# Kernel tuning notes

Hardware: AMD Instinct MI355X
Metric: run time of the kernel (lower is better)

Reference implementation:

```python
import jax, jax.numpy as jnp
import numpy as np

EPS = 1e-10


def setup_inputs() -> dict:
    key = jax.random.key(0)
    k1, k2, k3 = jax.random.split(key, 3)
    B, c = 65536, 64
    xyz = jax.random.normal(k1, (B, 3, 1), dtype=jnp.float32)          # group centers
    xyz_group = xyz + 0.1 * jax.random.normal(k2, (B, 3, c), dtype=jnp.float32)  # neighbor points
    r_lrf = 0.2 + 0.8 * jax.random.uniform(k3, (B,), dtype=jnp.float32)  # per-group support radius
    return {"xyz": xyz, "xyz_group": xyz_group, "r_lrf": r_lrf}


def reference(xyz, xyz_group, r_lrf):
    # xyz: [B,3,1] center; xyz_group: [B,3,c] neighbors; r_lrf: [B]
    B, _, c = xyz_group.shape
    x = xyz - xyz_group                                   # [B,3,c]
    xxt = jnp.einsum('bic,bjc->bij', x, x) / c            # [B,3,3] covariance
    _, _, vh = jnp.linalg.svd(xxt)                        # vh: [B,3,3]
    v_last = vh[:, -1, :]                                 # [B,3] smallest singular vector (torch v[...,-1])

    # sign disambiguation (no-grad in the original)
    center_proj = jnp.einsum('bi,bic->bc', v_last, x)     # [B,c]
    sum_ = (center_proj > 0.001).sum(-1) - (center_proj < -0.001).sum(-1)  # [B]
    sign = jax.lax.stop_gradient(1.0 - 2.0 * (sum_ < 0).astype(jnp.float32))  # [B]

    zp = sign[:, None] * v_last                           # [B,3] z axis
    x = -x                                                # x *= -1 in original
    norm = jnp.einsum('bi,bic->bc', zp, x)                # [B,c] projection onto zp
    vi = x - zp[:, :, None] * norm[:, None, :]            # [B,3,c] in-plane component
    x_l2 = jnp.sqrt(jnp.sum(x * x, axis=1))               # [B,c]
    alpha = (r_lrf[:, None] - x_l2) ** 2                  # [B,c]
    beta = norm * norm                                    # [B,c]
    vi_c = jnp.einsum('bc,bic->bi', alpha * beta, vi)     # [B,3] weighted sum
    xp = vi_c / (jnp.sqrt(jnp.sum(vi_c * vi_c, axis=1, keepdims=True)) + EPS)  # [B,3] x axis
    yp = jnp.cross(xp, zp)                                # [B,3] y axis
    lrf = jnp.stack([xp, yp, zp], axis=2)                 # [B,3,3] columns = axes
    out = jnp.einsum('bij,bic->bjc', lrf, (xyz_group - xyz) / r_lrf[:, None, None])  # lrf^T @ _out_xp
    return out


if __name__ == '__main__':
    o = reference(**setup_inputs())
    print(o.shape)
```

## Files before the change

### kernel.cpp

```cpp
#include <hip/hip_runtime.h>


#define DEVFN static __device__ __forceinline__

DEVFN float frcp(float x) { return __builtin_amdgcn_rcpf(x); }
DEVFN float frsq(float x) { return __builtin_amdgcn_rsqf(x); }


DEVFN float slapy2f(float x, float y) {
#pragma clang fp contract(off)
  float xa = fabsf(x), ya = fabsf(y);
  float w = fmaxf(xa, ya);
  float z = fminf(xa, ya);
  if (z == 0.0f) return w;
  float q = z / w;
  return w * sqrtf(fmaf(q, q, 1.0f));
}

DEVFN float snrm2_2f(float a, float b) {
  double da = (double)a, db = (double)b;
  return (float)sqrt(da * da + db * db);
}

DEVFN void slartgf(float f, float g, float &cs, float &sn, float &r) {
#pragma clang fp contract(off)
  if (g == 0.0f) { cs = 1.0f; sn = 0.0f; r = f; return; }
  if (f == 0.0f) { cs = 0.0f; sn = copysignf(1.0f, g); r = fabsf(g); return; }
  float f1 = fabsf(f), g1 = fabsf(g);
  const float rtmin = 0x1p-63f;
  const float rtmax = 6.5219089e18f;
  if (f1 > rtmin && f1 < rtmax && g1 > rtmin && g1 < rtmax) {
    float d = sqrtf(fmaf(f, f, g * g));
    cs = f1 / d;
    r = copysignf(d, f);
    sn = g / r;
  } else {
    const float safmin = 0x1p-126f;
    const float safmax = 0x1p+126f;
    float u = fminf(safmax, fmaxf(safmin, fmaxf(f1, g1)));
    float fs = f / u, gs = g / u;
    float d = sqrtf(fmaf(fs, fs, gs * gs));
    cs = fabsf(fs) / d;
    r = copysignf(d, f);
    sn = gs / r;
    r = r * u;
  }
}

DEVFN void slas2f(float f, float g, float h, float &ssmin, float &ssmax) {
#pragma clang fp contract(off)
  float fa = fabsf(f), ga = fabsf(g), ha = fabsf(h);
  float fhmn = fminf(fa, ha), fhmx = fmaxf(fa, ha);
  if (fhmn == 0.0f) {
    ssmin = 0.0f;
    if (fhmx == 0.0f) {
      ssmax = ga;
    } else {
      float mx = fmaxf(fhmx, ga), mn = fminf(fhmx, ga);
      float q = mn / mx;
      ssmax = mx * sqrtf(fmaf(q, q, 1.0f));
    }
  } else {
    if (ga < fhmx) {
      float as = 1.0f + fhmn / fhmx;
      float at = (fhmx - fhmn) / fhmx;
      float qq = ga / fhmx;
      float au = qq * qq;
      float c = 2.0f / (sqrtf(fmaf(as, as, au)) + sqrtf(fmaf(at, at, au)));
      ssmin = fhmn * c;
      ssmax = fhmx / c;
    } else {
      float au = fhmx / ga;
      if (au == 0.0f) {
        ssmin = (fhmn * fhmx) / ga;
        ssmax = ga;
      } else {
        float as = 1.0f + fhmn / fhmx;
        float at = (fhmx - fhmn) / fhmx;
        float q1 = as * au, q2 = at * au;
        float c = 1.0f / (sqrtf(fmaf(q1, q1, 1.0f)) + sqrtf(fmaf(q2, q2, 1.0f)));
        ssmin = (fhmn * c) * au;
        ssmin = ssmin + ssmin;
        ssmax = ga / (c + c);
      }
    }
  }
}

DEVFN void slasv2f(float f, float g, float h, float &ssmin, float &ssmax,
                   float &snr, float &csr, float &snl, float &csl) {
#pragma clang fp contract(off)
  const float eps = 0x1p-24f;
  float ft = f, fa = fabsf(f), ht = h, ha = fabsf(h);
  int pmax = 1;
  bool swp = (ha > fa);
  if (swp) {
    pmax = 3;
    float tmp = ft; ft = ht; ht = tmp;
    tmp = fa; fa = ha; ha = tmp;
  }
  float gt = g, ga = fabsf(g);
  float clt = 0.0f, crt = 0.0f, slt = 0.0f, srt = 0.0f;
  if (ga == 0.0f) {
    ssmin = ha; ssmax = fa;
    clt = 1.0f; crt = 1.0f; slt = 0.0f; srt = 0.0f;
  } else {
    bool gasmal = true;
    if (ga > fa) {
      pmax = 2;
      if ((fa / ga) < eps) {
        gasmal = false;
        ssmax = ga;
        if (ha > 1.0f) ssmin = fa / (ga / ha);
        else ssmin = (fa / ga) * ha;
        clt = 1.0f; slt = ht / gt; srt = 1.0f; crt = ft / gt;
      }
    }
    if (gasmal) {
      float dd = fa - ha;
      float l;
      if (dd == fa) l = 1.0f;
      else l = dd / fa;
      float m = gt / ft;
      float t = 2.0f - l;
      float s = sqrtf(fmaf(m, m, t * t));
      float r;
      if (l == 0.0f) r = fabsf(m);
      else r = sqrtf(fmaf(m, m, l * l));
      float a = 0.5f * (s + r);
      ssmin = ha / a;
      ssmax = fa * a;
      float mm = m * m;
      if (mm == 0.0f) {
        if (l == 0.0f) t = copysignf(2.0f, ft) * copysignf(1.0f, gt);
        else t = gt / copysignf(dd, ft) + m / t;
      } else {
        t = (m / (s + t) + m / (r + l)) * (1.0f + a);
      }
      float l2 = sqrtf(fmaf(t, t, 4.0f));
      crt = 2.0f / l2;
      srt = t / l2;
      clt = fmaf(srt, m, crt) / a;
      slt = (ht / ft) * srt / a;
    }
  }
  if (swp) { csl = srt; snl = crt; csr = slt; snr = clt; }
  else { csl = clt; snl = slt; csr = crt; snr = srt; }
  float tsign = 0.0f;
  if (pmax == 1) tsign = copysignf(1.0f, csr) * copysignf(1.0f, csl) * copysignf(1.0f, f);
  if (pmax == 2) tsign = copysignf(1.0f, snr) * copysignf(1.0f, csl) * copysignf(1.0f, g);
  if (pmax == 3) tsign = copysignf(1.0f, snr) * copysignf(1.0f, snl) * copysignf(1.0f, h);
  ssmax = copysignf(ssmax, tsign);
  ssmin = copysignf(ssmin, tsign * copysignf(1.0f, f) * copysignf(1.0f, h));
}

#define GROT(hi1, hi2, hi3, lo1, lo2, lo3, ct_, st_)          \
  do {                                                        \
    float c__ = (ct_), s__ = (st_);                           \
    if (c__ != 1.0f || s__ != 0.0f) {                         \
      float t_;                                               \
      t_ = hi1; hi1 = fmaf(c__, t_, -(s__ * lo1)); lo1 = fmaf(s__, t_, c__ * lo1); \
      t_ = hi2; hi2 = fmaf(c__, t_, -(s__ * lo2)); lo2 = fmaf(s__, t_, c__ * lo2); \
      t_ = hi3; hi3 = fmaf(c__, t_, -(s__ * lo3)); lo3 = fmaf(s__, t_, c__ * lo3); \
    }                                                         \
  } while (0)

#define ROT2X2(lo1, lo2, lo3, hi1, hi2, hi3, cr_, sr_)        \
  do {                                                        \
    float xx_, yy_, st_;                                      \
    xx_ = lo1; yy_ = hi1; st_ = fmaf(cr_, xx_, sr_ * yy_);    \
    hi1 = fmaf(cr_, yy_, -(sr_ * xx_)); lo1 = st_;            \
    xx_ = lo2; yy_ = hi2; st_ = fmaf(cr_, xx_, sr_ * yy_);    \
    hi2 = fmaf(cr_, yy_, -(sr_ * xx_)); lo2 = st_;            \
    xx_ = lo3; yy_ = hi3; st_ = fmaf(cr_, xx_, sr_ * yy_);    \
    hi3 = fmaf(cr_, yy_, -(sr_ * xx_)); lo3 = st_;            \
  } while (0)

#define VSWAP(a, b) { float t_ = (a); (a) = (b); (b) = t_; }

static __device__ void svd3_vlast(float c00, float c01, float c02,
                                  float c11, float c12, float c22,
                                  float vout[3]) {
#pragma clang fp contract(off)
  float a11 = c00, a12 = c01, a13 = c02;
  float a21 = c01, a22 = c11, a23 = c12;
  float a31 = c02, a32 = c12, a33 = c22;
  float d1, d2, d3, e1, e2;
  float taup1 = 0.0f, g2 = 0.0f;

  {
    float xnorm = snrm2_2f(a21, a31);
    if (xnorm == 0.0f) {
      d1 = a11;
    } else {
      float beta = -copysignf(slapy2f(a11, xnorm), a11);
      float tauq1 = (beta - a11) / beta;
      float sc = 1.0f / (a11 - beta);
      float v2 = a21 * sc, v3 = a31 * sc;
      d1 = beta;
      float w2 = fmaf(a32, v3, a22 * v2);
      float w3 = fmaf(a33, v3, a23 * v2);
      w2 = w2 + a12;
      w3 = w3 + a13;
      a12 = fmaf(-tauq1, w2, a12);
      a13 = fmaf(-tauq1, w3, a13);
      float t2 = -tauq1 * w2;
      float t3 = -tauq1 * w3;
      a22 = fmaf(v2, t2, a22); a32 = fmaf(v3, t2, a32);
      a23 = fmaf(v2, t3, a23); a33 = fmaf(v3, t3, a33);
    }
  }
  {
    float xnorm = fabsf(a13);
    if (xnorm == 0.0f) {
      e1 = a12;
    } else {
      float beta = -copysignf(slapy2f(a12, xnorm), a12);
      taup1 = (beta - a12) / beta;
      g2 = a13 * (1.0f / (a12 - beta));
      e1 = beta;
      float w2 = a23 * g2;
      float w3 = a33 * g2;
      w2 = w2 + a22;
      w3 = w3 + a32;
      a22 = fmaf(-taup1, w2, a22);
      a32 = fmaf(-taup1, w3, a32);
      float tg = -taup1 * g2;
      a23 = fmaf(w2, tg, a23);
      a33 = fmaf(w3, tg, a33);
    }
  }
  {
    float xnorm = fabsf(a32);
    if (xnorm == 0.0f) {
      d2 = a22;
    } else {
      float beta = -copysignf(slapy2f(a22, xnorm), a22);
      float tauq2 = (beta - a22) / beta;
      float h3 = a32 * (1.0f / (a22 - beta));
      d2 = beta;
      float w = a33 * h3;
      w = w + a23;
      a23 = fmaf(-tauq2, w, a23);
      float tw = -tauq2 * w;
      a33 = fmaf(h3, tw, a33);
    }
  }
  e2 = a23;
  d3 = a33;

  float vt11 = 1.0f, vt12 = 0.0f, vt13 = 0.0f;
  float vt21 = 0.0f, vt22 = 1.0f, vt23 = 0.0f;
  float vt31 = 0.0f, vt32 = 0.0f, vt33 = 1.0f;

  const float eps = 0x1p-24f;
  const float unfl = 0x1p-126f;
  const float tol = 10.0f * eps;
  float thresh;
  {
    float sminoa = fabsf(d1);
    if (sminoa != 0.0f) {
      float mu = sminoa;
      mu = fabsf(d2) * (mu / (mu + fabsf(e1)));
      sminoa = fminf(sminoa, mu);
      if (sminoa != 0.0f) {
        mu = fabsf(d3) * (mu / (mu + fabsf(e2)));
        sminoa = fminf(sminoa, mu);
      }
    }
    sminoa = sminoa / sqrtf(3.0f);
    thresh = fmaxf(tol * sminoa, 6.0f * (3.0f * (3.0f * unfl)));
  }
  int mq = 3;
  int iterq = -1, iterdivn = 0;
  const int maxitdivn = 18;
  int oldll = -1, oldm = -1, idir = 0;
  float sminl = 0.0f;
  int guard = 0;

  while (true) {
    if (mq <= 1) break;
    if (++guard > 300) break;
    if (iterq >= 3) {
      iterq -= 3;
      iterdivn += 1;
      if (iterdivn >= maxitdivn) break;
    }
    if (mq == 2) {
      if (fabsf(e1) <= thresh) { e1 = 0.0f; mq = 1; continue; }
      float sigmn, sigmx, sinr, cosr, sinl, cosl;
      slasv2f(d1, e1, d2, sigmn, sigmx, sinr, cosr, sinl, cosl);
      d1 = sigmx; e1 = 0.0f; d2 = sigmn;
      ROT2X2(vt11, vt12, vt13, vt21, vt22, vt23, cosr, sinr);
      mq = 0;
      continue;
    }
    float smax = fabsf(d3);
    if (fabsf(e2) <= thresh) { e2 = 0.0f; mq = 2; continue; }
    smax = fmaxf(fmaxf(smax, fabsf(d2)), fabsf(e2));
    if (fabsf(e1) <= thresh) {
      e1 = 0.0f;
      float sigmn, sigmx, sinr, cosr, sinl, cosl;
      slasv2f(d2, e2, d3, sigmn, sigmx, sinr, cosr, sinl, cosl);
      d2 = sigmx; e2 = 0.0f; d3 = sigmn;
      ROT2X2(vt21, vt22, vt23, vt31, vt32, vt33, cosr, sinr);
      mq = 1;
      continue;
    }
    smax = fmaxf(fmaxf(smax, fabsf(d1)), fabsf(e1));
    if (1 > oldm || 3 < oldll)
      idir = (fabsf(d1) >= fabsf(d3)) ? 1 : 2;
    bool back = false;
    if (idir == 1) {
      if (fabsf(e2) <= tol * fabsf(d3)) { e2 = 0.0f; continue; }
      float mu = fabsf(d1);
      sminl = mu;
      if (fabsf(e1) <= tol * mu) { e1 = 0.0f; back = true; }
      else {
        mu = fabsf(d2) * (mu / (mu + fabsf(e1)));
        sminl = fminf(sminl, mu);
        if (fabsf(e2) <= tol * mu) { e2 = 0.0f; back = true; }
        else {
          mu = fabsf(d3) * (mu / (mu + fabsf(e2)));
          sminl = fminf(sminl, mu);
        }
      }
    } else {
      if (fabsf(e1) <= tol * fabsf(d1)) { e1 = 0.0f; continue; }
      float mu = fabsf(d3);
      sminl = mu;
      if (fabsf(e2) <= tol * mu) { e2 = 0.0f; back = true; }
      else {
        mu = fabsf(d2) * (mu / (mu + fabsf(e2)));
        sminl = fminf(sminl, mu);
        if (fabsf(e1) <= tol * mu) { e1 = 0.0f; back = true; }
        else {
          mu = fabsf(d1) * (mu / (mu + fabsf(e1)));
          sminl = fminf(sminl, mu);
        }
      }
    }
    if (back) continue;
    oldll = 1;
    oldm = 3;
    float shift = 0.0f;
    if (!((3.0f * tol) * (sminl / smax) <= fmaxf(eps, 0.01f * tol))) {
      float sll, rdum;
      if (idir == 1) { sll = fabsf(d1); slas2f(d2, e2, d3, shift, rdum); }
      else { sll = fabsf(d3); slas2f(d1, e1, d2, shift, rdum); }
      if (sll > 0.0f) {
        float q = shift / sll;
        if (q * q < eps) shift = 0.0f;
      }
    }
    iterq += 2;
    float rc0, rc1, rs0, rs1;
    if (shift == 0.0f) {
      if (idir == 1) {
        float cs = 1.0f, oldcs = 1.0f, sn = 0.0f, oldsn = 0.0f, rr = 0.0f;
        float fq = d1 * cs;
        slartgf(fq, e1, cs, sn, rr);
        float f2 = oldcs * rr;
        float g2q = d2 * sn;
        slartgf(f2, g2q, oldcs, oldsn, d1);
        rc0 = cs; rs0 = sn;
        fq = d2 * cs;
        slartgf(fq, e2, cs, sn, rr);
        e1 = oldsn * rr;
        f2 = oldcs * rr;
        g2q = d3 * sn;
        slartgf(f2, g2q, oldcs, oldsn, d2);
        rc1 = cs; rs1 = sn;
        float h = d3 * cs;
        d3 = h * oldcs;
        e2 = h * oldsn;
        GROT(vt21, vt22, vt23, vt11, vt12, vt13, rc0, rs0);
        GROT(vt31, vt32, vt33, vt21, vt22, vt23, rc1, rs1);
        if (fabsf(e2) <= thresh) e2 = 0.0f;
      } else {
        float cs = 1.0f, oldcs = 1.0f, sn = 0.0f, oldsn = 0.0f, rr = 0.0f;
        float fq = d3 * cs;
        slartgf(fq, e2, cs, sn, rr);
        float f2 = oldcs * rr;
        float g2q = d2 * sn;
        slartgf(f2, g2q, oldcs, oldsn, d3);
        rc1 = oldcs; rs1 = -oldsn;
        fq = d2 * cs;
        slartgf(fq, e1, cs, sn, rr);
        e2 = oldsn * rr;
        f2 = oldcs * rr;
        g2q = d1 * sn;
        slartgf(f2, g2q, oldcs, oldsn, d2);
        rc0 = oldcs; rs0 = -oldsn;
        float h = d1 * cs;
        d1 = h * oldcs;
        e1 = h * oldsn;
        GROT(vt31, vt32, vt33, vt21, vt22, vt23, rc1, rs1);
        GROT(vt21, vt22, vt23, vt11, vt12, vt13, rc0, rs0);
        if (fabsf(e1) <= thresh) e1 = 0.0f;
      }
    } else {
      if (idir == 1) {
        float fq = (fabsf(d1) - shift) * (copysignf(1.0f, d1) + shift / d1);
        float gq = e1;
        float cosr = 0, sinr = 0, cosl = 0, sinl = 0, rr = 0;
        slartgf(fq, gq, cosr, sinr, rr);
        fq = fmaf(cosr, d1, sinr * e1);
        e1 = fmaf(cosr, e1, -(sinr * d1));
        gq = sinr * d2;
        d2 = cosr * d2;
        slartgf(fq, gq, cosl, sinl, rr);
        d1 = rr;
        fq = fmaf(cosl, e1, sinl * d2);
        d2 = fmaf(cosl, d2, -(sinl * e1));
        gq = sinl * e2;
        e2 = cosl * e2;
        rc0 = cosr; rs0 = sinr;
        slartgf(fq, gq, cosr, sinr, rr);
        e1 = rr;
        fq = fmaf(cosr, d2, sinr * e2);
        e2 = fmaf(cosr, e2, -(sinr * d2));
        gq = sinr * d3;
        d3 = cosr * d3;
        slartgf(fq, gq, cosl, sinl, rr);
        d2 = rr;
        fq = fmaf(cosl, e2, sinl * d3);
        d3 = fmaf(cosl, d3, -(sinl * e2));
        rc1 = cosr; rs1 = sinr;
        e2 = fq;
        GROT(vt21, vt22, vt23, vt11, vt12, vt13, rc0, rs0);
        GROT(vt31, vt32, vt33, vt21, vt22, vt23, rc1, rs1);
        if (fabsf(e2) <= thresh) e2 = 0.0f;
      } else {
        float fq = (fabsf(d3) - shift) * (copysignf(1.0f, d3) + shift / d3);
        float gq = e2;
        float cosr = 0, sinr = 0, cosl = 0, sinl = 0, rr = 0;
        slartgf(fq, gq, cosr, sinr, rr);
        fq = fmaf(cosr, d3, sinr * e2);
        e2 = fmaf(cosr, e2, -(sinr * d3));
        gq = sinr * d2;
        d2 = cosr * d2;
        slartgf(fq, gq, cosl, sinl, rr);
        d3 = rr;
        fq = fmaf(cosl, e2, sinl * d2);
        d2 = fmaf(cosl, d2, -(sinl * e2));
        gq = sinl * e1;
        e1 = cosl * e1;
        rc1 = cosl; rs1 = -sinl;
        slartgf(fq, gq, cosr, sinr, rr);
        e2 = rr;
        fq = fmaf(cosr, d2, sinr * e1);
        e1 = fmaf(cosr, e1, -(sinr * d2));
        gq = sinr * d1;
        d1 = cosr * d1;
        slartgf(fq, gq, cosl, sinl, rr);
        d2 = rr;
        fq = fmaf(cosl, e1, sinl * d1);
        d1 = fmaf(cosl, d1, -(sinl * e1));
        rc0 = cosl; rs0 = -sinl;
        e1 = fq;
        if (fabsf(e1) <= thresh) e1 = 0.0f;
        GROT(vt31, vt32, vt33, vt21, vt22, vt23, rc1, rs1);
        GROT(vt21, vt22, vt23, vt11, vt12, vt13, rc0, rs0);
      }
    }
  }
  if (d1 < 0.0f) { d1 = -d1; vt11 = -vt11; vt12 = -vt12; vt13 = -vt13; }
  if (d2 < 0.0f) { d2 = -d2; vt21 = -vt21; vt22 = -vt22; vt23 = -vt23; }
  if (d3 < 0.0f) { d3 = -d3; vt31 = -vt31; vt32 = -vt32; vt33 = -vt33; }
  {
    int isub = 1; float smin = d1;
    if (d2 <= smin) { isub = 2; smin = d2; }
    if (d3 <= smin) { isub = 3; smin = d3; }
    if (isub != 3) {
      if (isub == 1) {
        d1 = d3; d3 = smin;
        VSWAP(vt11, vt31); VSWAP(vt12, vt32); VSWAP(vt13, vt33);
      } else {
        d2 = d3; d3 = smin;
        VSWAP(vt21, vt31); VSWAP(vt22, vt32); VSWAP(vt23, vt33);
      }
    }
  }
  {
    int isub = 1; float smin = d1;
    if (d2 <= smin) { isub = 2; smin = d2; }
    if (isub != 2) {
      d1 = d2; d2 = smin;
      VSWAP(vt11, vt21); VSWAP(vt12, vt22); VSWAP(vt13, vt23);
    }
  }
  float r1 = vt31, r2 = vt32, r3 = vt33;
  if (taup1 != 0.0f) {
    float w = r3 * g2;
    w = w + r2;
    r2 = fmaf(-taup1, w, r2);
    float tg = -taup1 * g2;
    r3 = fmaf(w, tg, r3);
  }
  vout[0] = r1;
  vout[1] = r2;
  vout[2] = r3;
}


#define JSWAPF(a, b) { float t_ = (a); (a) = (b); (b) = t_; }

DEVFN void jacobi3f(float a00, float a01, float a02,
                    float a11, float a12, float a22,
                    float vmin[3], float u2o[3], float &lmax, float &gap) {
  float v00 = 1.0f, v01 = 0.0f, v02 = 0.0f;
  float v10 = 0.0f, v11 = 1.0f, v12 = 0.0f;
  float v20 = 0.0f, v21 = 0.0f, v22 = 1.0f;

#pragma unroll
  for (int sweep = 0; sweep < 5; ++sweep) {
    if (a01 != 0.0f) {
      float tau = (a11 - a00) * 0.5f * frcp(a01);
      float t = copysignf(1.0f, tau) * frcp(fabsf(tau) + sqrtf(fmaf(tau, tau, 1.0f)));
      float c = frsq(fmaf(t, t, 1.0f));
      float s = t * c;
      float old01 = a01;
      a00 = a00 - t * old01;
      a11 = a11 + t * old01;
      a01 = 0.0f;
      float n02 = c * a02 - s * a12;
      float n12 = s * a02 + c * a12;
      a02 = n02; a12 = n12;
      float x;
      x = v00; v00 = c * x - s * v01; v01 = s * x + c * v01;
      x = v10; v10 = c * x - s * v11; v11 = s * x + c * v11;
      x = v20; v20 = c * x - s * v21; v21 = s * x + c * v21;
    }
    if (a02 != 0.0f) {
      float tau = (a22 - a00) * 0.5f * frcp(a02);
      float t = copysignf(1.0f, tau) * frcp(fabsf(tau) + sqrtf(fmaf(tau, tau, 1.0f)));
      float c = frsq(fmaf(t, t, 1.0f));
      float s = t * c;
      float old02 = a02;
      a00 = a00 - t * old02;
      a22 = a22 + t * old02;
      a02 = 0.0f;
      float n01 = c * a01 - s * a12;
      float n12 = s * a01 + c * a12;
      a01 = n01; a12 = n12;
      float x;
      x = v00; v00 = c * x - s * v02; v02 = s * x + c * v02;
      x = v10; v10 = c * x - s * v12; v12 = s * x + c * v12;
      x = v20; v20 = c * x - s * v22; v22 = s * x + c * v22;
    }
    if (a12 != 0.0f) {
      float tau = (a22 - a11) * 0.5f * frcp(a12);
      float t = copysignf(1.0f, tau) * frcp(fabsf(tau) + sqrtf(fmaf(tau, tau, 1.0f)));
      float c = frsq(fmaf(t, t, 1.0f));
      float s = t * c;
      float old12 = a12;
      a11 = a11 - t * old12;
      a22 = a22 + t * old12;
      a12 = 0.0f;
      float n01 = c * a01 - s * a02;
      float n02 = s * a01 + c * a02;
      a01 = n01; a02 = n02;
      float x;
      x = v01; v01 = c * x - s * v02; v02 = s * x + c * v02;
      x = v11; v11 = c * x - s * v12; v12 = s * x + c * v12;
      x = v21; v21 = c * x - s * v22; v22 = s * x + c * v22;
    }
  }

  float L0 = a00, L1 = a11, L2 = a22;
  if (L0 < L1) { JSWAPF(L0, L1); JSWAPF(v00, v01); JSWAPF(v10, v11); JSWAPF(v20, v21); }
  if (L0 < L2) { JSWAPF(L0, L2); JSWAPF(v00, v02); JSWAPF(v10, v12); JSWAPF(v20, v22); }
  if (L1 < L2) { JSWAPF(L1, L2); JSWAPF(v01, v02); JSWAPF(v11, v12); JSWAPF(v21, v22); }
  lmax = L0;
  gap = L1 - L2;

  float n2 = frsq(v02 * v02 + v12 * v12 + v22 * v22);
  vmin[0] = v02 * n2;
  vmin[1] = v12 * n2;
  vmin[2] = v22 * n2;
  float n1 = frsq(v01 * v01 + v11 * v11 + v21 * v21);
  u2o[0] = v01 * n1;
  u2o[1] = v11 * n1;
  u2o[2] = v21 * n1;
}

DEVFN float qsum(float x) {
#pragma clang fp contract(off)
  float s = x + __shfl_xor(x, 1);
  return s + __shfl_xor(s, 2);
}
DEVFN int qsumi(int x) {
  int s = x + __shfl_xor(x, 1);
  return s + __shfl_xor(s, 2);
}

#define CHAIN4(acc, A, Bv)            \
  do {                                \
    float t_ = A[3] * Bv[3] + acc;    \
    t_ = A[2] * Bv[2] + t_;           \
    t_ = A[1] * Bv[1] + t_;           \
    acc = A[0] * Bv[0] + t_;          \
  } while (0)

#define PASS3(Z0, Z1, Z2, OVX, OVY, OVZ)                      \
  do {                                                        \
    float vx = 0, vy = 0, vz = 0;                             \
    _Pragma("unroll")                                         \
    for (int Bk = 0; Bk < 4; ++Bk) {                          \
      float w[4], q0[4], q1[4], q2[4];                        \
      _Pragma("unroll")                                       \
      for (int j = 0; j < 4; ++j) {                           \
        int i = 4 * Bk + j;                                   \
        float y0 = r0[i] - cx;                                \
        float y1 = r1[i] - cy;                                \
        float y2 = r2[i] - cz;                                \
        float nm = (Z0) * y0;                                 \
        nm = (Z1) * y1 + nm;                                  \
        nm = (Z2) * y2 + nm;                                  \
        q0[j] = y0 - (Z0) * nm;                               \
        q1[j] = y1 - (Z1) * nm;                               \
        q2[j] = y2 - (Z2) * nm;                               \
        float ss_ = y0 * y0;                                  \
        ss_ = ss_ + y1 * y1;                                  \
        ss_ = ss_ + y2 * y2;                                  \
        float xl2_ = sqrtf(ss_);                              \
        float am_ = r - xl2_;                                 \
        float alpha_ = am_ * am_;                             \
        float beta_ = nm * nm;                                \
        w[j] = alpha_ * beta_;                                \
      }                                                       \
      CHAIN4(vx, w, q0);                                      \
      CHAIN4(vy, w, q1);                                      \
      CHAIN4(vz, w, q2);                                      \
    }                                                         \
    OVX = qsum(vx);                                           \
    OVY = qsum(vy);                                           \
    OVZ = qsum(vz);                                           \
  } while (0)


__global__ __launch_bounds__(256)
__attribute__((amdgpu_waves_per_eu(2, 4)))
void LRF_70695161692718_main(
    const float* __restrict__ xyz, const float* __restrict__ xyzg,
    const float* __restrict__ rl, float* __restrict__ out,
    float* __restrict__ covws, int* __restrict__ cnt, int* __restrict__ list,
    int B) {
#pragma clang fp contract(off)
  int tid = blockIdx.x * blockDim.x + threadIdx.x;
  int b = tid >> 2;
  int l = tid & 3;
  if (b >= B) return;
  const float* Xg = xyzg + (size_t)b * 192;
  float cx = xyz[3 * b + 0], cy = xyz[3 * b + 1], cz = xyz[3 * b + 2];
  float r = rl[b];

  float r0[16], r1[16], r2[16];
#pragma unroll
  for (int i = 0; i < 16; ++i) {
    int col = 4 * i + l;
    r0[i] = Xg[col];
    r1[i] = Xg[64 + col];
    r2[i] = Xg[128 + col];
  }

  float a00 = 0, a01 = 0, a02 = 0, a11 = 0, a12 = 0, a22 = 0;
#pragma unroll
  for (int Bk = 0; Bk < 4; ++Bk) {
    float x0[4], x1[4], x2[4];
#pragma unroll
    for (int j = 0; j < 4; ++j) {
      int i = 4 * Bk + j;
      x0[j] = cx - r0[i];
      x1[j] = cy - r1[i];
      x2[j] = cz - r2[i];
    }
    CHAIN4(a00, x0, x0);
    CHAIN4(a01, x0, x1);
    CHAIN4(a02, x0, x2);
    CHAIN4(a11, x1, x1);
    CHAIN4(a12, x1, x2);
    CHAIN4(a22, x2, x2);
  }
  a00 = qsum(a00) / 64.0f;
  a01 = qsum(a01) / 64.0f;
  a02 = qsum(a02) / 64.0f;
  a11 = qsum(a11) / 64.0f;
  a12 = qsum(a12) / 64.0f;
  a22 = qsum(a22) / 64.0f;

  float v[3], u2[3];
  float lmax, gap;
  jacobi3f(a00, a01, a02, a11, a12, a22, v, u2, lmax, gap);

  int flag = !(gap > 0.032f * lmax);

  const float MARG2 = 9.61e-10f;
  int npos = 0, nneg = 0, nshk = 0;
#pragma unroll
  for (int i = 0; i < 16; ++i) {
    float x0 = cx - r0[i];
    float x1 = cy - r1[i];
    float x2 = cz - r2[i];
    float p = v[0] * x0;
    p = v[1] * x1 + p;
    p = v[2] * x2 + p;
    float ss_ = x0 * x0;
    ss_ = ss_ + x1 * x1;
    ss_ = ss_ + x2 * x2;
    float d = fabsf(fabsf(p) - 0.001f);
    npos += (p > 0.001f) ? 1 : 0;
    nneg += (p < -0.001f) ? 1 : 0;
    nshk += (d * d <= MARG2 * ss_) ? 1 : 0;
  }
  int sum_ = qsumi(npos) - qsumi(nneg);
  int nsh = qsumi(nshk);
  flag |= (sum_ >= -nsh) && (sum_ <= nsh);

  float sgn = (sum_ < 0) ? -1.0f : 1.0f;
  float zp0 = sgn * v[0], zp1 = sgn * v[1], zp2 = sgn * v[2];

  float vx = 0, vy = 0, vz = 0;
  float dAx = 0, dAy = 0, dAz = 0, dSm = 0, dSnm = 0;
#pragma unroll
  for (int Bk = 0; Bk < 4; ++Bk) {
    float w[4], q0[4], q1[4], q2[4];
#pragma unroll
    for (int j = 0; j < 4; ++j) {
      int i = 4 * Bk + j;
      float y0 = r0[i] - cx;
      float y1 = r1[i] - cy;
      float y2 = r2[i] - cz;
      float nm = zp0 * y0;
      nm = zp1 * y1 + nm;
      nm = zp2 * y2 + nm;
      q0[j] = y0 - zp0 * nm;
      q1[j] = y1 - zp1 * nm;
      q2[j] = y2 - zp2 * nm;
      float ss_ = y0 * y0;
      ss_ = ss_ + y1 * y1;
      ss_ = ss_ + y2 * y2;
      float xl2_ = sqrtf(ss_);
      float am_ = r - xl2_;
      float alpha_ = am_ * am_;
      float beta_ = nm * nm;
      w[j] = alpha_ * beta_;
      float m = u2[0] * y0;
      m = u2[1] * y1 + m;
      m = u2[2] * y2 + m;
      float g2m = 2.0f * alpha_ * nm * m;
      dAx = fmaf(g2m, q0[j], dAx);
      dAy = fmaf(g2m, q1[j], dAy);
      dAz = fmaf(g2m, q2[j], dAz);
      dSm = fmaf(w[j], m, dSm);
      dSnm = fmaf(w[j], nm, dSnm);
    }
    CHAIN4(vx, w, q0);
    CHAIN4(vy, w, q1);
    CHAIN4(vz, w, q2);
  }
  float vcx = qsum(vx);
  float vcy = qsum(vy);
  float vcz = qsum(vz);
  float Ax = qsum(dAx);
  float Ay = qsum(dAy);
  float Az = qsum(dAz);
  float Sm = qsum(dSm);
  float Snm = qsum(dSnm);

  float Dx = Ax - Sm * zp0 - Snm * u2[0];
  float Dy = Ay - Sm * zp1 - Snm * u2[1];
  float Dz = Az - Sm * zp2 - Snm * u2[2];
  float D2 = Dx * Dx + Dy * Dy + Dz * Dz;

  float ss = vcx * vcx;
  ss = ss + vcy * vcy;
  ss = ss + vcz * vcz;
  float vnorm = sqrtf(ss);
  float den = vnorm + 1e-10f;
  float xp0 = vcx / den, xp1 = vcy / den, xp2 = vcz / den;

  flag |= !(9e-10f * D2 < 2.89e-6f * ss);

  float yp0 = xp1 * zp2 - xp2 * zp1;
  float yp1 = xp2 * zp0 - xp0 * zp2;
  float yp2 = xp0 * zp1 - xp1 * zp0;

  if (flag) {
    if (l == 0) {
      float* s = covws + (size_t)b * 6;
      s[0] = a00; s[1] = a01; s[2] = a02;
      s[3] = a11; s[4] = a12; s[5] = a22;
      int pos = atomicAdd(cnt, 1);
      list[pos] = b;
    }
    return;
  }

  float* O = out + (size_t)b * 192;
#pragma unroll
  for (int i = 0; i < 16; ++i) {
    int col = 4 * i + l;
    float y0 = r0[i] - cx;
    float y1 = r1[i] - cy;
    float y2 = r2[i] - cz;
    float p0 = y0 / r, p1 = y1 / r, p2 = y2 / r;
    float t0 = xp0 * p0; t0 = xp1 * p1 + t0; t0 = xp2 * p2 + t0;
    float t1 = yp0 * p0; t1 = yp1 * p1 + t1; t1 = yp2 * p2 + t1;
    float t2 = zp0 * p0; t2 = zp1 * p1 + t2; t2 = zp2 * p2 + t2;
    O[col] = t0;
    O[64 + col] = t1;
    O[128 + col] = t2;
  }
}


__global__ __launch_bounds__(256)
__attribute__((amdgpu_waves_per_eu(2, 4)))
void LRF_70695161692718_fix(
    const float* __restrict__ xyz, const float* __restrict__ xyzg,
    const float* __restrict__ rl, float* __restrict__ out,
    const float* __restrict__ covws, const int* __restrict__ cnt,
    const int* __restrict__ list, int B) {
#pragma clang fp contract(off)
  int tid = blockIdx.x * blockDim.x + threadIdx.x;
  int idx = tid >> 2;
  int l = tid & 3;
  int n = *cnt;
  if (idx >= n) return;
  int b = list[idx];

  const float* s = covws + (size_t)b * 6;
  float a00 = s[0], a01 = s[1], a02 = s[2];
  float a11 = s[3], a12 = s[4], a22 = s[5];

  float v[3];
  svd3_vlast(a00, a01, a02, a11, a12, a22, v);

  const float* Xg = xyzg + (size_t)b * 192;
  float cx = xyz[3 * b + 0], cy = xyz[3 * b + 1], cz = xyz[3 * b + 2];
  float r = rl[b];

  float r0[16], r1[16], r2[16];
#pragma unroll
  for (int i = 0; i < 16; ++i) {
    int col = 4 * i + l;
    r0[i] = Xg[col];
    r1[i] = Xg[64 + col];
    r2[i] = Xg[128 + col];
  }

  int npos = 0, nneg = 0;
#pragma unroll
  for (int i = 0; i < 16; ++i) {
    float x0 = cx - r0[i];
    float x1 = cy - r1[i];
    float x2 = cz - r2[i];
    float p = v[0] * x0;
    p = v[1] * x1 + p;
    p = v[2] * x2 + p;
    npos += (p > 0.001f) ? 1 : 0;
    nneg += (p < -0.001f) ? 1 : 0;
  }
  int sum_ = qsumi(npos) - qsumi(nneg);
  float sgn = (sum_ < 0) ? -1.0f : 1.0f;
  float zp0 = sgn * v[0], zp1 = sgn * v[1], zp2 = sgn * v[2];

  float vcx, vcy, vcz;
  PASS3(zp0, zp1, zp2, vcx, vcy, vcz);
  float ss = vcx * vcx;
  ss = ss + vcy * vcy;
  ss = ss + vcz * vcz;
  float den = sqrtf(ss) + 1e-10f;
  float xp0 = vcx / den, xp1 = vcy / den, xp2 = vcz / den;
  float yp0 = xp1 * zp2 - xp2 * zp1;
  float yp1 = xp2 * zp0 - xp0 * zp2;
  float yp2 = xp0 * zp1 - xp1 * zp0;

  float* O = out + (size_t)b * 192;
#pragma unroll
  for (int i = 0; i < 16; ++i) {
    int col = 4 * i + l;
    float y0 = r0[i] - cx;
    float y1 = r1[i] - cy;
    float y2 = r2[i] - cz;
    float p0 = y0 / r, p1 = y1 / r, p2 = y2 / r;
    float t0 = xp0 * p0; t0 = xp1 * p1 + t0; t0 = xp2 * p2 + t0;
    float t1 = yp0 * p0; t1 = yp1 * p1 + t1; t1 = yp2 * p2 + t1;
    float t2 = zp0 * p0; t2 = zp1 * p1 + t2; t2 = zp2 * p2 + t2;
    O[col] = t0;
    O[64 + col] = t1;
    O[128 + col] = t2;
  }
}


__global__ __launch_bounds__(256)
__attribute__((amdgpu_waves_per_eu(2, 4)))
void LRF_70695161692718_mono(
    const float* __restrict__ xyz, const float* __restrict__ xyzg,
    const float* __restrict__ rl, float* __restrict__ out, int B) {
#pragma clang fp contract(off)
  int tid = blockIdx.x * blockDim.x + threadIdx.x;
  int b = tid >> 2;
  int l = tid & 3;
  if (b >= B) return;
  const float* Xg = xyzg + (size_t)b * 192;
  float cx = xyz[3 * b + 0], cy = xyz[3 * b + 1], cz = xyz[3 * b + 2];
  float r = rl[b];

  float r0[16], r1[16], r2[16];
#pragma unroll
  for (int i = 0; i < 16; ++i) {
    int col = 4 * i + l;
    r0[i] = Xg[col];
    r1[i] = Xg[64 + col];
    r2[i] = Xg[128 + col];
  }

  float a00 = 0, a01 = 0, a02 = 0, a11 = 0, a12 = 0, a22 = 0;
#pragma unroll
  for (int Bk = 0; Bk < 4; ++Bk) {
    float x0[4], x1[4], x2[4];
#pragma unroll
    for (int j = 0; j < 4; ++j) {
      int i = 4 * Bk + j;
      x0[j] = cx - r0[i];
      x1[j] = cy - r1[i];
      x2[j] = cz - r2[i];
    }
    CHAIN4(a00, x0, x0);
    CHAIN4(a01, x0, x1);
    CHAIN4(a02, x0, x2);
    CHAIN4(a11, x1, x1);
    CHAIN4(a12, x1, x2);
    CHAIN4(a22, x2, x2);
  }
  a00 = qsum(a00) / 64.0f;
  a01 = qsum(a01) / 64.0f;
  a02 = qsum(a02) / 64.0f;
  a11 = qsum(a11) / 64.0f;
  a12 = qsum(a12) / 64.0f;
  a22 = qsum(a22) / 64.0f;

  float v[3];
  svd3_vlast(a00, a01, a02, a11, a12, a22, v);

  int npos = 0, nneg = 0;
#pragma unroll
  for (int i = 0; i < 16; ++i) {
    float x0 = cx - r0[i];
    float x1 = cy - r1[i];
    float x2 = cz - r2[i];
    float p = v[0] * x0;
    p = v[1] * x1 + p;
    p = v[2] * x2 + p;
    npos += (p > 0.001f) ? 1 : 0;
    nneg += (p < -0.001f) ? 1 : 0;
  }
  int sum_ = qsumi(npos) - qsumi(nneg);
  float sgn = (sum_ < 0) ? -1.0f : 1.0f;
  float zp0 = sgn * v[0], zp1 = sgn * v[1], zp2 = sgn * v[2];

  float vcx, vcy, vcz;
  PASS3(zp0, zp1, zp2, vcx, vcy, vcz);
  float ss = vcx * vcx;
  ss = ss + vcy * vcy;
  ss = ss + vcz * vcz;
  float den = sqrtf(ss) + 1e-10f;
  float xp0 = vcx / den, xp1 = vcy / den, xp2 = vcz / den;
  float yp0 = xp1 * zp2 - xp2 * zp1;
  float yp1 = xp2 * zp0 - xp0 * zp2;
  float yp2 = xp0 * zp1 - xp1 * zp0;

  float* O = out + (size_t)b * 192;
#pragma unroll
  for (int i = 0; i < 16; ++i) {
    int col = 4 * i + l;
    float y0 = r0[i] - cx;
    float y1 = r1[i] - cy;
    float y2 = r2[i] - cz;
    float p0 = y0 / r, p1 = y1 / r, p2 = y2 / r;
    float t0 = xp0 * p0; t0 = xp1 * p1 + t0; t0 = xp2 * p2 + t0;
    float t1 = yp0 * p0; t1 = yp1 * p1 + t1; t1 = yp2 * p2 + t1;
    float t2 = zp0 * p0; t2 = zp1 * p1 + t2; t2 = zp2 * p2 + t2;
    O[col] = t0;
    O[64 + col] = t1;
    O[128 + col] = t2;
  }
}

extern "C" void kernel_launch(void* const* d_in, const int* in_sizes, int n_in,
                              void* d_out, int out_size, void* d_ws, size_t ws_size,
                              hipStream_t stream) {
  (void)n_in; (void)out_size;
  const float* xyz = (const float*)d_in[0];
  const float* xyzg = (const float*)d_in[1];
  const float* rl = (const float*)d_in[2];
  float* out = (float*)d_out;
  int B = in_sizes[2];
  int blocks = (B * 4 + 255) / 256;

  size_t need = (size_t)B * 24 + 64 + (size_t)B * 4;
  if (d_ws != nullptr && ws_size >= need) {
    float* covws = (float*)d_ws;
    int* cnt = (int*)((char*)d_ws + (size_t)B * 24);
    int* list = cnt + 16;
    hipMemsetAsync(cnt, 0, 4, stream);
    LRF_70695161692718_main<<<blocks, 256, 0, stream>>>(
        xyz, xyzg, rl, out, covws, cnt, list, B);
    LRF_70695161692718_fix<<<blocks, 256, 0, stream>>>(
        xyz, xyzg, rl, out, covws, cnt, list, B);
  } else {
    LRF_70695161692718_mono<<<blocks, 256, 0, stream>>>(xyz, xyzg, rl, out, B);
  }
}
```

Measured before the change: 156.7 us.

## Vectorize main kernel loads/stores with float4 and drop covariance workspace

The main kernel now gives each of the 4 lanes per group a contiguous 16-column slab loaded and stored as float4, in place of strided scalar accesses. It also drops the fp-contract-off pragma and CHAIN4 ordering so the compiler can fuse into FMAs, and replaces divisions with reciprocal multiplies. The covariance workspace is removed: the fix kernel recomputes the covariance from the input points instead of reading it back. The risk is small numerical differences from FMA contraction and a different summation order, which could change which groups get flagged for the slow fix path.

```diff
diff --git a/kernel.cpp b/kernel.cpp
--- a/kernel.cpp
+++ b/kernel.cpp
@@ -645,44 +645,33 @@
 void LRF_70695161692718_main(
     const float* __restrict__ xyz, const float* __restrict__ xyzg,
     const float* __restrict__ rl, float* __restrict__ out,
-    float* __restrict__ covws, int* __restrict__ cnt, int* __restrict__ list,
-    int B) {
-#pragma clang fp contract(off)
+    int* __restrict__ cnt, int* __restrict__ list, int B) {
   int tid = blockIdx.x * blockDim.x + threadIdx.x;
   int b = tid >> 2;
   int l = tid & 3;
   if (b >= B) return;
-  const float* Xg = xyzg + (size_t)b * 192;
   float cx = xyz[3 * b + 0], cy = xyz[3 * b + 1], cz = xyz[3 * b + 2];
   float r = rl[b];
 
-  float r0[16], r1[16], r2[16];
-#pragma unroll
-  for (int i = 0; i < 16; ++i) {
-    int col = 4 * i + l;
-    r0[i] = Xg[col];
-    r1[i] = Xg[64 + col];
-    r2[i] = Xg[128 + col];
+  const float4* G = (const float4*)(xyzg + (size_t)b * 192);
+  float4 R0[4], R1[4], R2[4];
+#pragma unroll
+  for (int j = 0; j < 4; ++j) {
+    R0[j] = G[4 * l + j];
+    R1[j] = G[16 + 4 * l + j];
+    R2[j] = G[32 + 4 * l + j];
   }
 
   float a00 = 0, a01 = 0, a02 = 0, a11 = 0, a12 = 0, a22 = 0;
-#pragma unroll
-  for (int Bk = 0; Bk < 4; ++Bk) {
-    float x0[4], x1[4], x2[4];
-#pragma unroll
-    for (int j = 0; j < 4; ++j) {
-      int i = 4 * Bk + j;
-      x0[j] = cx - r0[i];
-      x1[j] = cy - r1[i];
-      x2[j] = cz - r2[i];
-    }
-    CHAIN4(a00, x0, x0);
-    CHAIN4(a01, x0, x1);
-    CHAIN4(a02, x0, x2);
-    CHAIN4(a11, x1, x1);
-    CHAIN4(a12, x1, x2);
-    CHAIN4(a22, x2, x2);
-  }
+#define COV_C(C)                                              \
+  {                                                           \
+    float x0 = cx - R0[j].C, x1 = cy - R1[j].C, x2 = cz - R2[j].C; \
+    a00 += x0 * x0; a01 += x0 * x1; a02 += x0 * x2;           \
+    a11 += x1 * x1; a12 += x1 * x2; a22 += x2 * x2;           \
+  }
+#pragma unroll
+  for (int j = 0; j < 4; ++j) { COV_C(x) COV_C(y) COV_C(z) COV_C(w) }
+#undef COV_C
   a00 = qsum(a00) / 64.0f;
   a01 = qsum(a01) / 64.0f;
   a02 = qsum(a02) / 64.0f;
@@ -698,22 +687,19 @@
 
   const float MARG2 = 9.61e-10f;
   int npos = 0, nneg = 0, nshk = 0;
-#pragma unroll
-  for (int i = 0; i < 16; ++i) {
-    float x0 = cx - r0[i];
-    float x1 = cy - r1[i];
-    float x2 = cz - r2[i];
-    float p = v[0] * x0;
-    p = v[1] * x1 + p;
-    p = v[2] * x2 + p;
-    float ss_ = x0 * x0;
-    ss_ = ss_ + x1 * x1;
-    ss_ = ss_ + x2 * x2;
-    float d = fabsf(fabsf(p) - 0.001f);
-    npos += (p > 0.001f) ? 1 : 0;
-    nneg += (p < -0.001f) ? 1 : 0;
-    nshk += (d * d <= MARG2 * ss_) ? 1 : 0;
-  }
+#define P2_C(C)                                               \
+  {                                                           \
+    float x0 = cx - R0[j].C, x1 = cy - R1[j].C, x2 = cz - R2[j].C; \
+    float p = x0 * v[0] + x1 * v[1] + x2 * v[2];              \
+    float sseg = x0 * x0 + x1 * x1 + x2 * x2;                 \
+    float d = fabsf(fabsf(p) - 0.001f);                       \
+    npos += (p > 0.001f) ? 1 : 0;                             \
+    nneg += (p < -0.001f) ? 1 : 0;                            \
+    nshk += (d * d <= MARG2 * sseg) ? 1 : 0;                  \
+  }
+#pragma unroll
+  for (int j = 0; j < 4; ++j) { P2_C(x) P2_C(y) P2_C(z) P2_C(w) }
+#undef P2_C
   int sum_ = qsumi(npos) - qsumi(nneg);
   int nsh = qsumi(nshk);
   flag |= (sum_ >= -nsh) && (sum_ <= nsh);
@@ -723,43 +709,26 @@
 
   float vx = 0, vy = 0, vz = 0;
   float dAx = 0, dAy = 0, dAz = 0, dSm = 0, dSnm = 0;
-#pragma unroll
-  for (int Bk = 0; Bk < 4; ++Bk) {
-    float w[4], q0[4], q1[4], q2[4];
-#pragma unroll
-    for (int j = 0; j < 4; ++j) {
-      int i = 4 * Bk + j;
-      float y0 = r0[i] - cx;
-      float y1 = r1[i] - cy;
-      float y2 = r2[i] - cz;
-      float nm = zp0 * y0;
-      nm = zp1 * y1 + nm;
-      nm = zp2 * y2 + nm;
-      q0[j] = y0 - zp0 * nm;
-      q1[j] = y1 - zp1 * nm;
-      q2[j] = y2 - zp2 * nm;
-      float ss_ = y0 * y0;
-      ss_ = ss_ + y1 * y1;
-      ss_ = ss_ + y2 * y2;
-      float xl2_ = sqrtf(ss_);
-      float am_ = r - xl2_;
-      float alpha_ = am_ * am_;
-      float beta_ = nm * nm;
-      w[j] = alpha_ * beta_;
-      float m = u2[0] * y0;
-      m = u2[1] * y1 + m;
-      m = u2[2] * y2 + m;
-      float g2m = 2.0f * alpha_ * nm * m;
-      dAx = fmaf(g2m, q0[j], dAx);
-      dAy = fmaf(g2m, q1[j], dAy);
-      dAz = fmaf(g2m, q2[j], dAz);
-      dSm = fmaf(w[j], m, dSm);
-      dSnm = fmaf(w[j], nm, dSnm);
-    }
-    CHAIN4(vx, w, q0);
-    CHAIN4(vy, w, q1);
-    CHAIN4(vz, w, q2);
-  }
+#define P3_C(C)                                               \
+  {                                                           \
+    float y0 = R0[j].C - cx, y1 = R1[j].C - cy, y2 = R2[j].C - cz; \
+    float nm = zp0 * y0 + zp1 * y1 + zp2 * y2;                \
+    float q0 = y0 - zp0 * nm;                                 \
+    float q1 = y1 - zp1 * nm;                                 \
+    float q2 = y2 - zp2 * nm;                                 \
+    float sseg = y0 * y0 + y1 * y1 + y2 * y2;                 \
+    float am = r - sqrtf(sseg);                               \
+    float alpha = am * am;                                    \
+    float w = alpha * (nm * nm);                              \
+    vx += w * q0; vy += w * q1; vz += w * q2;                 \
+    float m = u2[0] * y0 + u2[1] * y1 + u2[2] * y2;           \
+    float g2m = 2.0f * alpha * nm * m;                        \
+    dAx += g2m * q0; dAy += g2m * q1; dAz += g2m * q2;        \
+    dSm += w * m; dSnm += w * nm;                             \
+  }
+#pragma unroll
+  for (int j = 0; j < 4; ++j) { P3_C(x) P3_C(y) P3_C(z) P3_C(w) }
+#undef P3_C
   float vcx = qsum(vx);
   float vcy = qsum(vy);
   float vcz = qsum(vz);
@@ -774,12 +743,9 @@
   float Dz = Az - Sm * zp2 - Snm * u2[2];
   float D2 = Dx * Dx + Dy * Dy + Dz * Dz;
 
-  float ss = vcx * vcx;
-  ss = ss + vcy * vcy;
-  ss = ss + vcz * vcz;
-  float vnorm = sqrtf(ss);
-  float den = vnorm + 1e-10f;
-  float xp0 = vcx / den, xp1 = vcy / den, xp2 = vcz / den;
+  float ss = vcx * vcx + vcy * vcy + vcz * vcz;
+  float dinv = frcp(sqrtf(ss) + 1e-10f);
+  float xp0 = vcx * dinv, xp1 = vcy * dinv, xp2 = vcz * dinv;
 
   flag |= !(9e-10f * D2 < 2.89e-6f * ss);
 
@@ -789,29 +755,31 @@
 
   if (flag) {
     if (l == 0) {
-      float* s = covws + (size_t)b * 6;
-      s[0] = a00; s[1] = a01; s[2] = a02;
-      s[3] = a11; s[4] = a12; s[5] = a22;
       int pos = atomicAdd(cnt, 1);
       list[pos] = b;
     }
     return;
   }
 
-  float* O = out + (size_t)b * 192;
-#pragma unroll
-  for (int i = 0; i < 16; ++i) {
-    int col = 4 * i + l;
-    float y0 = r0[i] - cx;
-    float y1 = r1[i] - cy;
-    float y2 = r2[i] - cz;
-    float p0 = y0 / r, p1 = y1 / r, p2 = y2 / r;
-    float t0 = xp0 * p0; t0 = xp1 * p1 + t0; t0 = xp2 * p2 + t0;
-    float t1 = yp0 * p0; t1 = yp1 * p1 + t1; t1 = yp2 * p2 + t1;
-    float t2 = zp0 * p0; t2 = zp1 * p1 + t2; t2 = zp2 * p2 + t2;
-    O[col] = t0;
-    O[64 + col] = t1;
-    O[128 + col] = t2;
+  float rinv = frcp(r);
+  float4* Ov = (float4*)(out + (size_t)b * 192);
+#pragma unroll
+  for (int j = 0; j < 4; ++j) {
+    float4 o0, o1, o2;
+#define P4_C(C)                                               \
+    {                                                         \
+      float p0 = (R0[j].C - cx) * rinv;                       \
+      float p1 = (R1[j].C - cy) * rinv;                       \
+      float p2 = (R2[j].C - cz) * rinv;                       \
+      o0.C = xp0 * p0 + xp1 * p1 + xp2 * p2;                  \
+      o1.C = yp0 * p0 + yp1 * p1 + yp2 * p2;                  \
+      o2.C = zp0 * p0 + zp1 * p1 + zp2 * p2;                  \
+    }
+    P4_C(x) P4_C(y) P4_C(z) P4_C(w)
+#undef P4_C
+    Ov[4 * l + j] = o0;
+    Ov[16 + 4 * l + j] = o1;
+    Ov[32 + 4 * l + j] = o2;
   }
 }
 
@@ -821,8 +789,7 @@
 void LRF_70695161692718_fix(
     const float* __restrict__ xyz, const float* __restrict__ xyzg,
     const float* __restrict__ rl, float* __restrict__ out,
-    const float* __restrict__ covws, const int* __restrict__ cnt,
-    const int* __restrict__ list, int B) {
+    const int* __restrict__ cnt, const int* __restrict__ list, int B) {
 #pragma clang fp contract(off)
   int tid = blockIdx.x * blockDim.x + threadIdx.x;
   int idx = tid >> 2;
@@ -831,13 +798,6 @@
   if (idx >= n) return;
   int b = list[idx];
 
-  const float* s = covws + (size_t)b * 6;
-  float a00 = s[0], a01 = s[1], a02 = s[2];
-  float a11 = s[3], a12 = s[4], a22 = s[5];
-
-  float v[3];
-  svd3_vlast(a00, a01, a02, a11, a12, a22, v);
-
   const float* Xg = xyzg + (size_t)b * 192;
   float cx = xyz[3 * b + 0], cy = xyz[3 * b + 1], cz = xyz[3 * b + 2];
   float r = rl[b];
@@ -850,6 +810,34 @@
     r1[i] = Xg[64 + col];
     r2[i] = Xg[128 + col];
   }
+
+  float a00 = 0, a01 = 0, a02 = 0, a11 = 0, a12 = 0, a22 = 0;
+#pragma unroll
+  for (int Bk = 0; Bk < 4; ++Bk) {
+    float x0[4], x1[4], x2[4];
+#pragma unroll
+    for (int j = 0; j < 4; ++j) {
+      int i = 4 * Bk + j;
+      x0[j] = cx - r0[i];
+      x1[j] = cy - r1[i];
+      x2[j] = cz - r2[i];
+    }
+    CHAIN4(a00, x0, x0);
+    CHAIN4(a01, x0, x1);
+    CHAIN4(a02, x0, x2);
+    CHAIN4(a11, x1, x1);
+    CHAIN4(a12, x1, x2);
+    CHAIN4(a22, x2, x2);
+  }
+  a00 = qsum(a00) / 64.0f;
+  a01 = qsum(a01) / 64.0f;
+  a02 = qsum(a02) / 64.0f;
+  a11 = qsum(a11) / 64.0f;
+  a12 = qsum(a12) / 64.0f;
+  a22 = qsum(a22) / 64.0f;
+
+  float v[3];
+  svd3_vlast(a00, a01, a02, a11, a12, a22, v);
 
   int npos = 0, nneg = 0;
 #pragma unroll
@@ -1002,16 +990,15 @@
   int B = in_sizes[2];
   int blocks = (B * 4 + 255) / 256;
 
-  size_t need = (size_t)B * 24 + 64 + (size_t)B * 4;
+  size_t need = 64 + (size_t)B * 4;
   if (d_ws != nullptr && ws_size >= need) {
-    float* covws = (float*)d_ws;
-    int* cnt = (int*)((char*)d_ws + (size_t)B * 24);
+    int* cnt = (int*)d_ws;
     int* list = cnt + 16;
     hipMemsetAsync(cnt, 0, 4, stream);
     LRF_70695161692718_main<<<blocks, 256, 0, stream>>>(
-        xyz, xyzg, rl, out, covws, cnt, list, B);
+        xyz, xyzg, rl, out, cnt, list, B);
     LRF_70695161692718_fix<<<blocks, 256, 0, stream>>>(
-        xyz, xyzg, rl, out, covws, cnt, list, B);
+        xyz, xyzg, rl, out, cnt, list, B);
   } else {
     LRF_70695161692718_mono<<<blocks, 256, 0, stream>>>(xyz, xyzg, rl, out, B);
   }
```

New measurement: 156.2 us. About the same (-0.3%).
